# Performance work log

Measured on AMD Instinct MI355X. Metric: run time of the kernel, lower is better.

Reference implementation:

```python
import jax, jax.numpy as jnp
import numpy as np

# ---- constants from the source module ----
NB = [[0,1,2,3],[0,1,4],[0,2,5],[0,3,6],[1,4,7],[2,5,8],[3,6,9],[4,7,10],[5,8,11],[6,9],[7,10],[8,11],[12,13,14,15],[12,13,16],[12,14,17],[12,15],[13,16,18],[14,17,19],[16,18,20],[17,19,21],[18,20,22],[19,21,23],[20,22],[21,23]]
PARENT = np.array([0,0,0,0,1,2,3,4,5,6,7,8,9,9,9,12,13,14,16,17,18,19,20,21])  # root parent sentinel handled separately
KJ, NV, PREG = 24, 6890, 200
LEN = np.array([len(n) for n in NB])
NBR_IDX = np.zeros((KJ,4), np.int32)
NBR_VALID = np.zeros((KJ,4), np.float32)
for k, n in enumerate(NB):
    NBR_IDX[k,:len(n)] = n; NBR_VALID[k,:len(n)] = 1.0
BETA_POS = np.zeros((KJ,17), np.float32); BETA_POS[np.arange(KJ), 4*LEN] = 1.0
SLICE_MASK = np.zeros((23,17), np.float32)
for j in range(23):
    SLICE_MASK[j,:4*LEN[j]+1] = 1.0  # self.K[j] has 4*len(NB[j])+1 rows
NBR_IDX = jnp.asarray(NBR_IDX); NBR_VALID = jnp.asarray(NBR_VALID)
BETA_POS = jnp.asarray(BETA_POS); SLICE_MASK = jnpp = jnp.asarray(SLICE_MASK)


def setup_inputs() -> dict:
    key = jax.random.key(0)
    ks = jax.random.split(key, 9)
    V = jax.random.normal(ks[0], (PREG, NV, 3), jnp.float32)
    T = jax.random.normal(ks[1], (PREG, NV, 3), jnp.float32)
    J = jax.random.normal(ks[2], (PREG, KJ, 3), jnp.float32)
    theta = 0.3 * jax.random.normal(ks[3], (PREG, 72), jnp.float32)
    W_prime = jax.random.uniform(ks[4], (NV, KJ), jnp.float32)
    W_i = jax.random.uniform(ks[5], (NV, KJ), jnp.float32)
    W_i = W_i / W_i.sum(axis=1, keepdims=True)
    A = jax.random.uniform(ks[6], (23, NV), jnp.float32)
    K_mats = 0.01 * jax.random.normal(ks[7], (23, 17, 3 * NV), jnp.float32)
    K_mats = K_mats * SLICE_MASK[:, :, None]  # zero rows beyond the ragged per-joint size
    beta_2 = jnp.ones((1,), jnp.float32)
    return {"V": V, "T": T, "J": J, "theta": theta, "W_prime": W_prime, "W_i": W_i, "A": A, "K_mats": K_mats, "beta_2": beta_2, "epoch": 1}


def _rodrigues(pose):  # pose: (K,3)
    angle = jnp.maximum(jnp.linalg.norm(pose, axis=1, keepdims=True), 1e-8)
    axis = pose / angle
    x, y, z = axis[:, 0], axis[:, 1], axis[:, 2]
    zero = jnp.zeros_like(x)
    skew = jnp.stack([zero, -z, y, z, zero, -x, -y, x, zero], axis=1).reshape(-1, 3, 3)
    outer = axis[:, :, None] * axis[:, None, :]
    c = jnp.cos(angle)[:, :, None]
    s = jnp.sin(angle)[:, :, None]
    eye = jnp.eye(3, dtype=pose.dtype)[None]
    return c * eye + (1.0 - c) * outer + s * skew


def _compute_G(pose72, Jp):  # pose72: (72,), Jp: (K,3) -> (K,4,4)
    R = _rodrigues(pose72.reshape(KJ, 3))
    t = Jp - jnp.concatenate([jnp.zeros((1, 3), Jp.dtype), Jp[PARENT[1:]]], axis=0)
    G_local = jnp.zeros((KJ, 4, 4), Jp.dtype)
    G_local = G_local.at[:, :3, :3].set(R).at[:, :3, 3].set(t).at[:, 3, 3].set(1.0)
    Gs = [G_local[0]]
    for i in range(1, KJ):  # fixed 24-joint kinematic tree
        Gs.append(Gs[PARENT[i]] @ G_local[i])
    G = jnp.stack(Gs, axis=0)
    off = jnp.einsum('kij,kj->ki', G[:, :3, :3], Jp)  # homogeneous w=0 -> rotation only
    return G.at[:, :3, 3].add(-off)


def _axis2quat(p):  # (M,3) -> (M,4)
    angle = jnp.sqrt(jnp.maximum(jnp.sum(p ** 2, axis=1), 1e-16))
    n = p / angle[:, None]
    s = jnp.sin(angle / 2)
    return jnp.stack([n[:, 0] * s, n[:, 1] * s, n[:, 2] * s, jnp.cos(angle / 2) - 1.0], axis=1)


def reference(V, T, J, theta, W_prime, W_i, A, K_mats, beta_2, epoch):
    P = V.shape[0]
    b2 = beta_2[0]
    # normalized skinning weights
    W_relu = jax.nn.relu(W_prime)
    W_change = W_relu / (W_relu.sum(axis=1, keepdims=True) + 1e-8)
    # per-pose global joint transforms
    G_prime = jax.vmap(_compute_G)(theta, J)  # (P,K,4,4)
    # quaternion features and blend-shape correction
    q = _axis2quat(theta.reshape(P * KJ, 3)).reshape(P, KJ, 4)
    qg = q[:, NBR_IDX, :] * NBR_VALID[None, :, :, None]       # (P,K,4,4) neighbor gather
    q17 = jnp.concatenate([qg.reshape(P, KJ, 16), jnp.zeros((P, KJ, 1), q.dtype)], axis=-1)
    q17 = q17 + BETA_POS[None] * b2                            # beta_2 at column 4*len
    qm = q17[:, 1:, :] * SLICE_MASK[None]                      # ragged slice q_ne[:, j+1, :lenK]
    contrib = jnp.einsum('pjl,jlm->pjm', qm, K_mats).reshape(P, 23, NV, 3)
    T_p = jnp.einsum('pjnc,jn->pnc', contrib, jax.nn.relu(A)) + T
    # linear blend skinning
    T_h = jnp.concatenate([T_p, jnp.ones((P, NV, 1), T_p.dtype)], axis=-1)
    transformed = jnp.einsum('pkij,pnj->pnki', G_prime[:, :, :3, :], T_h)  # (P,N,K,3)
    verts = jnp.einsum('nk,pnkc->pnc', W_change, transformed)
    # energies
    e = float(epoch)
    g_wi = 0.1 * np.exp(-0.1 * e)
    g_w = 0.002 * np.exp(-0.008 * e)
    g_a = 0.001 * np.exp(-0.008 * e)
    g_k = 0.1 * np.exp(-0.008 * e)
    E_D = jnp.sum((V - verts) ** 2)
    E_Wi = jnp.sum((W_change - W_i) ** 2)
    E_W = jnp.sum(jnp.abs(W_change))
    E_A = jnp.sum(jnp.abs(A))
    E_K = jnp.sum(jnp.sqrt(jnp.sum(K_mats ** 2, axis=(1, 2))))
    E = E_D + g_wi * E_Wi + g_w * E_W + g_a * E_A + g_k * E_K
    return (E, verts)
```

## Files before the change

### kernel.cpp

```cpp
#include <hip/hip_runtime.h>
#include <math.h>

#define KJ 24
#define NV 6890
#define PREG 200
#define M_TOT (NV*3)
#define KDIM 391
#define KPAD 416
#define TP_STRIDE 20672
#define NMT64 323
#define NKB (NMT64*2)

#define EDP_OFF 0
#define EKP_OFF 5400
#define WIP_OFF 101984
#define EWP_OFF 102016
#define EAP_OFF 102048
#define RED_OFF 102080
#define G_OFF   102112
#define TP_OFF  159712
#define QBH_OFF_U 10903488
#define QBL_OFF_U 11009984
#define TP2_OFF 14157792

typedef __attribute__((ext_vector_type(8))) short short8;
typedef __attribute__((ext_vector_type(4))) float f32x4;
typedef __attribute__((ext_vector_type(4))) unsigned int u32x4;

__constant__ int c_PARENT[24] = {0,0,0,0,1,2,3,4,5,6,7,8,9,9,9,12,13,14,16,17,18,19,20,21};
__constant__ int c_DEPTH[24]  = {0,1,1,1,2,2,2,3,3,3,4,4,4,4,4,5,5,5,6,6,7,7,8,8};
__constant__ int c_LEN[24]    = {4,3,3,3,3,3,3,3,3,2,2,2,4,3,3,2,3,3,3,3,3,3,2,2};
__constant__ int c_NBR[24][4] = {
  {0,1,2,3},{0,1,4,0},{0,2,5,0},{0,3,6,0},{1,4,7,0},{2,5,8,0},{3,6,9,0},{4,7,10,0},
  {5,8,11,0},{6,9,0,0},{7,10,0,0},{8,11,0,0},{12,13,14,15},{12,13,16,0},{12,14,17,0},
  {12,15,0,0},{13,16,18,0},{14,17,19,0},{16,18,20,0},{17,19,21,0},{18,20,22,0},
  {19,21,23,0},{20,22,0,0},{21,23,0,0}};

__device__ __forceinline__ float waveReduce(float v) {
  #pragma unroll
  for (int off = 32; off > 0; off >>= 1) v += __shfl_down(v, off, 64);
  return v;
}
__device__ __forceinline__ unsigned short f2bf(float x) {
  union { float f; unsigned u; } v; v.f = x;
  unsigned r = v.u + 0x7FFFu + ((v.u >> 16) & 1u);
  return (unsigned short)(r >> 16);
}
__device__ __forceinline__ float bf2f(unsigned short h) {
  union { unsigned u; float f; } v; v.u = ((unsigned)h) << 16; return v.f;
}

__global__ __launch_bounds__(256) void kPre(const float* __restrict__ J,
                                            const float* __restrict__ theta,
                                            const float* __restrict__ beta2,
                                            const float* __restrict__ Wp,
                                            const float* __restrict__ Wi,
                                            const float* __restrict__ A,
                                            float* __restrict__ ws) {
  unsigned short* qbh = (unsigned short*)ws + QBH_OFF_U;
  unsigned short* qbl = (unsigned short*)ws + QBL_OFF_U;
  int b = blockIdx.x;
  if (b < 50) {
    __shared__ float Gl[4][24][12];
    __shared__ float Gg[4][24][12];
    __shared__ float q[4][24][4];
    int w = threadIdx.x >> 6, t = threadIdx.x & 63;
    int p = b*4 + w;
    if (t < 24) {
      float x = theta[p*72 + 3*t + 0];
      float y = theta[p*72 + 3*t + 1];
      float z = theta[p*72 + 3*t + 2];
      float n2 = x*x + y*y + z*z;
      float ang = fmaxf(sqrtf(n2), 1e-8f);
      float ia = 1.f/ang;
      float ax = x*ia, ay = y*ia, az = z*ia;
      float c = cosf(ang), s = sinf(ang), C = 1.f - c;
      float jx = J[p*72+3*t], jy = J[p*72+3*t+1], jz = J[p*72+3*t+2];
      float tx = jx, ty = jy, tz = jz;
      if (t > 0) {
        int par = c_PARENT[t];
        tx -= J[p*72+3*par]; ty -= J[p*72+3*par+1]; tz -= J[p*72+3*par+2];
      }
      Gl[w][t][0]=c+C*ax*ax;   Gl[w][t][1]=C*ax*ay-s*az; Gl[w][t][2]=C*ax*az+s*ay; Gl[w][t][3]=tx;
      Gl[w][t][4]=C*ax*ay+s*az;Gl[w][t][5]=c+C*ay*ay;    Gl[w][t][6]=C*ay*az-s*ax; Gl[w][t][7]=ty;
      Gl[w][t][8]=C*ax*az-s*ay;Gl[w][t][9]=C*ay*az+s*ax; Gl[w][t][10]=c+C*az*az;   Gl[w][t][11]=tz;
      float ang2 = sqrtf(fmaxf(n2, 1e-16f));
      float inv2 = 1.f/ang2;
      float s2 = sinf(0.5f*ang2);
      q[w][t][0] = x*inv2*s2; q[w][t][1] = y*inv2*s2; q[w][t][2] = z*inv2*s2;
      q[w][t][3] = cosf(0.5f*ang2) - 1.f;
    }
    __syncthreads();
    for (int lev = 0; lev <= 8; lev++) {
      if (t < 24 && c_DEPTH[t] == lev) {
        if (lev == 0) {
          for (int i2 = 0; i2 < 12; i2++) Gg[w][0][i2] = Gl[w][0][i2];
        } else {
          int par = c_PARENT[t];
          for (int r = 0; r < 3; r++) {
            float g0 = Gg[w][par][r*4+0], g1 = Gg[w][par][r*4+1];
            float g2 = Gg[w][par][r*4+2], g3 = Gg[w][par][r*4+3];
            for (int c2 = 0; c2 < 4; c2++) {
              float v = g0*Gl[w][t][0+c2] + g1*Gl[w][t][4+c2] + g2*Gl[w][t][8+c2];
              if (c2 == 3) v += g3;
              Gg[w][t][r*4+c2] = v;
            }
          }
        }
      }
      __syncthreads();
    }
    if (t < 24) {
      float jx = J[p*72+3*t], jy = J[p*72+3*t+1], jz = J[p*72+3*t+2];
      float* gp = ws + G_OFF + p*288 + t*12;
      #pragma unroll
      for (int r = 0; r < 3; r++) {
        float off = Gg[w][t][r*4+0]*jx + Gg[w][t][r*4+1]*jy + Gg[w][t][r*4+2]*jz;
        Gg[w][t][r*4+3] -= off;
      }
      #pragma unroll
      for (int i2 = 0; i2 < 12; i2++) gp[i2] = Gg[w][t][i2];
    }
    __syncthreads();
    float b2 = beta2[0];
    for (int e = t; e < KDIM; e += 64) {
      int j = e / 17, l = e - 17*j;
      int k = j + 1;
      float val = 0.f;
      if (l < 4*c_LEN[j] + 1) {
        if (l < 16) {
          int sidx = l >> 2, cc = l & 3;
          if (sidx < c_LEN[k]) val = q[w][c_NBR[k][sidx]][cc];
        }
        if (l == 4*c_LEN[k]) val += b2;
      }
      unsigned short hi = f2bf(val);
      unsigned short lo = f2bf(val - bf2f(hi));
      qbh[p*KPAD + e] = hi;
      qbl[p*KPAD + e] = lo;
    }
    for (int e = KDIM + t; e < KPAD; e += 64) {
      qbh[p*KPAD + e] = 0; qbl[p*KPAD + e] = 0;
    }
  } else {
    int d = b - 50;
    int t = threadIdx.x;
    int n = d*256 + t;
    float ewi = 0.f, ew = 0.f, ea = 0.f;
    if (n < NV) {
      float wv[24]; float sum = 0.f;
      const float4* wp4 = (const float4*)(Wp + n*24);
      #pragma unroll
      for (int i = 0; i < 6; i++) {
        float4 v4 = wp4[i];
        wv[4*i+0] = fmaxf(v4.x, 0.f); wv[4*i+1] = fmaxf(v4.y, 0.f);
        wv[4*i+2] = fmaxf(v4.z, 0.f); wv[4*i+3] = fmaxf(v4.w, 0.f);
        sum += wv[4*i+0]+wv[4*i+1]+wv[4*i+2]+wv[4*i+3];
      }
      float inv = 1.f/(sum + 1e-8f);
      #pragma unroll
      for (int k = 0; k < 24; k++) {
        float wc = wv[k]*inv;
        ew += fabsf(wc);
        float dd = wc - Wi[n*24+k];
        ewi += dd*dd;
      }
    }
    for (int i = d*256 + t; i < 23*NV; i += 27*256) ea += fabsf(A[i]);
    for (int i = d*256 + t; i < 56*KPAD; i += 27*256) {
      qbh[200*KPAD + i] = 0; qbl[200*KPAD + i] = 0;
    }
    __shared__ float red[3][4];
    int lane = t & 63, wv2 = t >> 6;
    ewi = waveReduce(ewi); ew = waveReduce(ew); ea = waveReduce(ea);
    if (lane == 0) { red[0][wv2] = ewi; red[1][wv2] = ew; red[2][wv2] = ea; }
    __syncthreads();
    if (t == 0) {
      ws[WIP_OFF + d] = red[0][0]+red[0][1]+red[0][2]+red[0][3];
      ws[EWP_OFF + d] = red[1][0]+red[1][1]+red[1][2]+red[1][3];
      ws[EAP_OFF + d] = red[2][0]+red[2][1]+red[2][2]+red[2][3];
    }
  }
}

template<int KS0, int NKS, int JMIN>
__device__ __forceinline__ void kb_body(const float* __restrict__ A,
                                        const float* __restrict__ K,
                                        const unsigned short* __restrict__ qbh,
                                        const unsigned short* __restrict__ qbl,
                                        float* __restrict__ Sk,
                                        short (*__restrict__ SBh)[64*32],
                                        short (*__restrict__ SBl)[64*32],
                                        float (*__restrict__ SA)[24],
                                        float* __restrict__ ek,
                                        float* __restrict__ ws,
                                        float* __restrict__ TPd,
                                        int m0, int flat) {
  const int tid = threadIdx.x;
  const int w = tid >> 6, lane = tid & 63;
  const int r = lane & 15, qd = lane >> 4;
  const int krow = tid >> 3, mseg = (tid & 7) * 8;
  const int mm = m0 + mseg;
  const int nb0 = m0 / 3;
  const int mrow2 = tid >> 2, kq2 = tid & 3;
  const int swr = ((mrow2 >> 4)*64 + kq2*16 + (mrow2 & 15)) * 8;

  if (tid < 23) ek[tid] = 0.f;
  for (int i = tid; i < 14*24; i += 256) {
    int jj = i / 24, nn = i - jj*24;
    int j2 = JMIN + jj, n2 = nb0 + nn;
    ((float*)SA)[i] = (j2 < 23 && n2 < NV) ? fmaxf(A[j2*NV + n2], 0.f) : 0.f;
  }

  f32x4 acc[4][4];
  #pragma unroll
  for (int h = 0; h < 4; h++)
    #pragma unroll
    for (int f = 0; f < 4; f++) acc[h][f] = (f32x4){0.f,0.f,0.f,0.f};

  int aofs[4];
  #pragma unroll
  for (int h = 0; h < 4; h++) aofs[h] = (w*64 + h*16 + r)*KPAD + KS0*32 + qd*8;

  short8 ah[2][4], al[2][4];
  float kv[8];

  auto loadK = [&](int ks) {
    int kg = (KS0 + ks)*32 + krow;
    #pragma unroll
    for (int i = 0; i < 8; i++) kv[i] = 0.f;
    if (kg < KDIM) {
      const float* kr = K + (size_t)kg*M_TOT + mm;
      if (mm + 7 < M_TOT) {
        float4 a4 = *(const float4*)kr; float4 b4 = *(const float4*)(kr+4);
        kv[0]=a4.x; kv[1]=a4.y; kv[2]=a4.z; kv[3]=a4.w;
        kv[4]=b4.x; kv[5]=b4.y; kv[6]=b4.z; kv[7]=b4.w;
      } else {
        #pragma unroll
        for (int i = 0; i < 8; i++) if (mm+i < M_TOT) kv[i] = kr[i];
      }
    }
  };
  auto stageK = [&](int ks) {
    int kg = (KS0 + ks)*32 + krow;
    float wv[8]; float sq = 0.f;
    #pragma unroll
    for (int i = 0; i < 8; i++) wv[i] = 0.f;
    if (kg < KDIM) {
      int jj = kg/17 - JMIN;
      int nb = mm / 3;
      float av[4];
      #pragma unroll
      for (int i = 0; i < 4; i++) av[i] = SA[jj][nb - nb0 + i];
      #pragma unroll
      for (int i = 0; i < 8; i++) {
        float a = (mm+i < M_TOT) ? av[(mm+i)/3 - nb] : 0.f;
        wv[i] = kv[i]*a;
        sq = fmaf(kv[i], kv[i], sq);
      }
    }
    #pragma unroll
    for (int c = 0; c < 4; c++)
      *(float2*)&Sk[krow*66 + mseg + 2*c] = make_float2(wv[2*c], wv[2*c+1]);
    sq += __shfl_xor(sq, 1, 64);
    sq += __shfl_xor(sq, 2, 64);
    sq += __shfl_xor(sq, 4, 64);
    if ((tid & 7) == 0 && kg < KDIM) atomicAdd(&ek[kg/17], sq);
  };
  auto xpose = [&](int buf) {
    float vv[8];
    #pragma unroll
    for (int j = 0; j < 8; j++) vv[j] = Sk[(kq2*8 + j)*66 + mrow2];
    unsigned dh[4], dl[4];
    #pragma unroll
    for (int c = 0; c < 4; c++) {
      unsigned short h0 = f2bf(vv[2*c]),   h1 = f2bf(vv[2*c+1]);
      unsigned short l0 = f2bf(vv[2*c]   - bf2f(h0));
      unsigned short l1 = f2bf(vv[2*c+1] - bf2f(h1));
      dh[c] = (unsigned)h0 | ((unsigned)h1 << 16);
      dl[c] = (unsigned)l0 | ((unsigned)l1 << 16);
    }
    *(u32x4*)&SBh[buf][swr] = (u32x4){dh[0], dh[1], dh[2], dh[3]};
    *(u32x4*)&SBl[buf][swr] = (u32x4){dl[0], dl[1], dl[2], dl[3]};
  };

  loadK(0);
  #pragma unroll
  for (int h = 0; h < 4; h++) {
    ah[0][h] = *(const short8*)(qbh + aofs[h]);
    al[0][h] = *(const short8*)(qbl + aofs[h]);
  }
  stageK(0);
  __syncthreads();
  xpose(0);
  #pragma unroll
  for (int h = 0; h < 4; h++) {
    ah[1][h] = *(const short8*)(qbh + aofs[h] + 32);
    al[1][h] = *(const short8*)(qbl + aofs[h] + 32);
  }
  __syncthreads();

  #pragma unroll
  for (int ks = 0; ks < NKS; ks++) {
    const int cur = ks & 1, nxt = cur ^ 1;
    if (ks + 1 < NKS) loadK(ks + 1);
    short8 bfh[4], bfl[4];
    #pragma unroll
    for (int f = 0; f < 4; f++) {
      bfh[f] = *(const short8*)&SBh[cur][(f*64 + lane)*8];
      bfl[f] = *(const short8*)&SBl[cur][(f*64 + lane)*8];
    }
    #pragma unroll
    for (int f = 0; f < 4; f++)
      #pragma unroll
      for (int h = 0; h < 4; h++) {
        acc[h][f] = __builtin_amdgcn_mfma_f32_16x16x32_bf16(ah[cur][h], bfh[f], acc[h][f], 0, 0, 0);
        acc[h][f] = __builtin_amdgcn_mfma_f32_16x16x32_bf16(ah[cur][h], bfl[f], acc[h][f], 0, 0, 0);
        acc[h][f] = __builtin_amdgcn_mfma_f32_16x16x32_bf16(al[cur][h], bfh[f], acc[h][f], 0, 0, 0);
      }
    if (ks + 1 < NKS) stageK(ks + 1);
    if (ks + 2 < NKS) {
      const int o = (ks + 2) * 32;
      #pragma unroll
      for (int h = 0; h < 4; h++) {
        ah[cur][h] = *(const short8*)(qbh + aofs[h] + o);
        al[cur][h] = *(const short8*)(qbl + aofs[h] + o);
      }
    }
    __syncthreads();
    if (ks + 1 < NKS) xpose(nxt);
    __syncthreads();
  }

  if (tid < 23) ws[EKP_OFF + tid*NKB + flat] = ek[tid];
  #pragma unroll
  for (int h = 0; h < 4; h++)
    #pragma unroll
    for (int f = 0; f < 4; f++)
      #pragma unroll
      for (int g = 0; g < 4; g++) {
        int p = w*64 + h*16 + qd*4 + g;
        if (p < PREG)
          TPd[(size_t)p*TP_STRIDE + m0 + f*16 + r] = acc[h][f][g];
      }
}

__global__ __launch_bounds__(256) void kB(const float* __restrict__ A,
                                          const float* __restrict__ K,
                                          float* __restrict__ ws) {
  __shared__ float Sk[32*66];
  __shared__ short SBh[2][64*32];
  __shared__ short SBl[2][64*32];
  __shared__ float SA[14][24];
  __shared__ float ek[23];
  const unsigned short* qbh = (const unsigned short*)ws + QBH_OFF_U;
  const unsigned short* qbl = (const unsigned short*)ws + QBL_OFF_U;
  const int m0 = blockIdx.x * 64;
  const int flat = blockIdx.x + blockIdx.y * NMT64;
  if (blockIdx.y == 0)
    kb_body<0, 7, 0>(A, K, qbh, qbl, Sk, SBh, SBl, SA, ek, ws, ws + TP_OFF,  m0, flat);
  else
    kb_body<7, 6, 13>(A, K, qbh, qbl, Sk, SBh, SBl, SA, ek, ws, ws + TP2_OFF, m0, flat);
}

__global__ __launch_bounds__(256) void kC(const float* __restrict__ V,
                                          const float* __restrict__ T,
                                          const float* __restrict__ Wp,
                                          const float* __restrict__ ws,
                                          float* __restrict__ out) {
  int p0 = blockIdx.y * 8;
  int n = blockIdx.x*256 + threadIdx.x;
  __shared__ float tmp[4];
  float ed = 0.f;
  if (n < NV) {
    float wv[24]; float sum = 0.f;
    const float4* wp4 = (const float4*)(Wp + n*24);
    #pragma unroll
    for (int i = 0; i < 6; i++) {
      float4 v4 = wp4[i];
      wv[4*i+0] = fmaxf(v4.x, 0.f); wv[4*i+1] = fmaxf(v4.y, 0.f);
      wv[4*i+2] = fmaxf(v4.z, 0.f); wv[4*i+3] = fmaxf(v4.w, 0.f);
      sum += wv[4*i+0]+wv[4*i+1]+wv[4*i+2]+wv[4*i+3];
    }
    float inv = 1.f/(sum + 1e-8f);
    for (int pp = 0; pp < 8; pp++) {
      int p = p0 + pp;
      const float* __restrict__ gp = ws + G_OFF + (size_t)p*288;
      float M[12];
      #pragma unroll
      for (int i = 0; i < 12; i++) M[i] = 0.f;
      #pragma unroll
      for (int k = 0; k < 24; k++) {
        float wc = wv[k];
        #pragma unroll
        for (int i = 0; i < 12; i++)
          M[i] = fmaf(wc, gp[k*12 + i], M[i]);
      }
      #pragma unroll
      for (int i = 0; i < 12; i++) M[i] *= inv;
      size_t tb = (size_t)p*M_TOT + 3*n;
      size_t pb = (size_t)p*TP_STRIDE + 3*n;
      float t0 = ws[TP_OFF + pb + 0] + ws[TP2_OFF + pb + 0] + T[tb + 0];
      float t1 = ws[TP_OFF + pb + 1] + ws[TP2_OFF + pb + 1] + T[tb + 1];
      float t2 = ws[TP_OFF + pb + 2] + ws[TP2_OFF + pb + 2] + T[tb + 2];
      float v0 = M[0]*t0 + M[1]*t1 + M[2]*t2  + M[3];
      float v1 = M[4]*t0 + M[5]*t1 + M[6]*t2  + M[7];
      float v2 = M[8]*t0 + M[9]*t1 + M[10]*t2 + M[11];
      out[1+tb+0] = v0; out[1+tb+1] = v1; out[1+tb+2] = v2;
      float d0 = V[tb+0]-v0, d1 = V[tb+1]-v1, d2 = V[tb+2]-v2;
      ed += d0*d0 + d1*d1 + d2*d2;
    }
  }
  ed = waveReduce(ed);
  int lane = threadIdx.x & 63, w = threadIdx.x >> 6;
  if (lane == 0) tmp[w] = ed;
  __syncthreads();
  if (threadIdx.x == 0)
    ((float*)ws)[EDP_OFF + blockIdx.y*27 + blockIdx.x] = tmp[0]+tmp[1]+tmp[2]+tmp[3];
}

__global__ __launch_bounds__(256) void kF1(float* __restrict__ ws) {
  __shared__ float sb[4];
  int b = blockIdx.x, t = threadIdx.x, lane = t & 63, w = t >> 6;
  if (b < 23) {
    float s = 0.f;
    for (int i = t; i < NKB; i += 256) s += ws[EKP_OFF + b*NKB + i];
    s = waveReduce(s);
    if (lane == 0) sb[w] = s;
    __syncthreads();
    if (t == 0) ws[RED_OFF + b] = sb[0]+sb[1]+sb[2]+sb[3];
  } else if (b == 23) {
    float s = 0.f;
    for (int i = t; i < 675; i += 256) s += ws[EDP_OFF + i];
    s = waveReduce(s);
    if (lane == 0) sb[w] = s;
    __syncthreads();
    if (t == 0) ws[RED_OFF + 23] = sb[0]+sb[1]+sb[2]+sb[3];
  } else {
    if (w == 0) {
      float s = (lane < 27) ? ws[WIP_OFF + lane] : 0.f;
      s = waveReduce(s);
      if (lane == 0) ws[RED_OFF + 24] = s;
    } else if (w == 1) {
      float s = (lane < 27) ? ws[EWP_OFF + lane] : 0.f;
      s = waveReduce(s);
      if (lane == 0) ws[RED_OFF + 25] = s;
    } else if (w == 2) {
      float s = (lane < 27) ? ws[EAP_OFF + lane] : 0.f;
      s = waveReduce(s);
      if (lane == 0) ws[RED_OFF + 26] = s;
    }
  }
}

__global__ void kF2(const int* __restrict__ epoch, const float* __restrict__ ws,
                    float* __restrict__ out) {
  int t = threadIdx.x;
  float s = (t < 23) ? sqrtf(ws[RED_OFF + t]) : 0.f;
  s = waveReduce(s);
  if (t == 0) {
    float e    = (float)epoch[0];
    float g_wi = 0.1f   * expf(-0.1f  * e);
    float g_w  = 0.002f * expf(-0.008f* e);
    float g_a  = 0.001f * expf(-0.008f* e);
    float g_k  = 0.1f   * expf(-0.008f* e);
    out[0] = ws[RED_OFF+23] + g_wi*ws[RED_OFF+24] + g_w*ws[RED_OFF+25]
           + g_a*ws[RED_OFF+26] + g_k*s;
  }
}

extern "C" void kernel_launch(void* const* d_in, const int* in_sizes, int n_in,
                              void* d_out, int out_size, void* d_ws, size_t ws_size,
                              hipStream_t stream) {
  const float* V     = (const float*)d_in[0];
  const float* T     = (const float*)d_in[1];
  const float* J     = (const float*)d_in[2];
  const float* theta = (const float*)d_in[3];
  const float* Wp    = (const float*)d_in[4];
  const float* Wi    = (const float*)d_in[5];
  const float* A     = (const float*)d_in[6];
  const float* K     = (const float*)d_in[7];
  const float* b2    = (const float*)d_in[8];
  const int*   epoch = (const int*)d_in[9];
  float* out = (float*)d_out;
  float* ws  = (float*)d_ws;

  hipLaunchKernelGGL(kPre, dim3(77),        dim3(256), 0, stream,
                     J, theta, b2, Wp, Wi, A, ws);
  hipLaunchKernelGGL(kB,   dim3(NMT64, 2),  dim3(256), 0, stream, A, K, ws);
  hipLaunchKernelGGL(kC,   dim3(27, 25),    dim3(256), 0, stream, V, T, Wp, ws, out);
  hipLaunchKernelGGL(kF1,  dim3(25),        dim3(256), 0, stream, ws);
  hipLaunchKernelGGL(kF2,  dim3(1),         dim3(64),  0, stream, epoch, ws, out);
}
```

Measured before the change: 175.6 us.

## Deepen kB pipeline with double-buffered staging and drop per-step barrier

The K-tile pipeline in kB becomes three stages deep: global loads run three steps ahead into a double-buffered register slot, staging runs two steps ahead into a double-buffered LDS scratch, and the transpose for the next step moves before the single remaining barrier, removing one __syncthreads per iteration. The per-joint norm accumulation no longer uses shared-memory atomics; each row's partial sum is written to LDS and reduced serially by 23 threads at the end. This costs more registers and LDS, which may lower occupancy, and the tail reduction loop is serial.

```diff
diff --git a/kernel.cpp b/kernel.cpp
--- a/kernel.cpp
+++ b/kernel.cpp
@@ -188,11 +188,11 @@
                                         const float* __restrict__ K,
                                         const unsigned short* __restrict__ qbh,
                                         const unsigned short* __restrict__ qbl,
-                                        float* __restrict__ Sk,
+                                        float (*__restrict__ Sk)[32*66],
                                         short (*__restrict__ SBh)[64*32],
                                         short (*__restrict__ SBl)[64*32],
                                         float (*__restrict__ SA)[24],
-                                        float* __restrict__ ek,
+                                        float* __restrict__ ek2,
                                         float* __restrict__ ws,
                                         float* __restrict__ TPd,
                                         int m0, int flat) {
@@ -205,7 +205,6 @@
   const int mrow2 = tid >> 2, kq2 = tid & 3;
   const int swr = ((mrow2 >> 4)*64 + kq2*16 + (mrow2 & 15)) * 8;
 
-  if (tid < 23) ek[tid] = 0.f;
   for (int i = tid; i < 14*24; i += 256) {
     int jj = i / 24, nn = i - jj*24;
     int j2 = JMIN + jj, n2 = nb0 + nn;
@@ -223,25 +222,27 @@
   for (int h = 0; h < 4; h++) aofs[h] = (w*64 + h*16 + r)*KPAD + KS0*32 + qd*8;
 
   short8 ah[2][4], al[2][4];
-  float kv[8];
+  float kv[2][8];
 
   auto loadK = [&](int ks) {
+    const int slot = ks & 1;
     int kg = (KS0 + ks)*32 + krow;
     #pragma unroll
-    for (int i = 0; i < 8; i++) kv[i] = 0.f;
+    for (int i = 0; i < 8; i++) kv[slot][i] = 0.f;
     if (kg < KDIM) {
       const float* kr = K + (size_t)kg*M_TOT + mm;
       if (mm + 7 < M_TOT) {
         float4 a4 = *(const float4*)kr; float4 b4 = *(const float4*)(kr+4);
-        kv[0]=a4.x; kv[1]=a4.y; kv[2]=a4.z; kv[3]=a4.w;
-        kv[4]=b4.x; kv[5]=b4.y; kv[6]=b4.z; kv[7]=b4.w;
+        kv[slot][0]=a4.x; kv[slot][1]=a4.y; kv[slot][2]=a4.z; kv[slot][3]=a4.w;
+        kv[slot][4]=b4.x; kv[slot][5]=b4.y; kv[slot][6]=b4.z; kv[slot][7]=b4.w;
       } else {
         #pragma unroll
-        for (int i = 0; i < 8; i++) if (mm+i < M_TOT) kv[i] = kr[i];
+        for (int i = 0; i < 8; i++) if (mm+i < M_TOT) kv[slot][i] = kr[i];
       }
     }
   };
   auto stageK = [&](int ks) {
+    const int slot = ks & 1;
     int kg = (KS0 + ks)*32 + krow;
     float wv[8]; float sq = 0.f;
     #pragma unroll
@@ -255,22 +256,23 @@
       #pragma unroll
       for (int i = 0; i < 8; i++) {
         float a = (mm+i < M_TOT) ? av[(mm+i)/3 - nb] : 0.f;
-        wv[i] = kv[i]*a;
-        sq = fmaf(kv[i], kv[i], sq);
+        wv[i] = kv[slot][i]*a;
+        sq = fmaf(kv[slot][i], kv[slot][i], sq);
       }
     }
     #pragma unroll
     for (int c = 0; c < 4; c++)
-      *(float2*)&Sk[krow*66 + mseg + 2*c] = make_float2(wv[2*c], wv[2*c+1]);
+      *(float2*)&Sk[slot][krow*66 + mseg + 2*c] = make_float2(wv[2*c], wv[2*c+1]);
     sq += __shfl_xor(sq, 1, 64);
     sq += __shfl_xor(sq, 2, 64);
     sq += __shfl_xor(sq, 4, 64);
-    if ((tid & 7) == 0 && kg < KDIM) atomicAdd(&ek[kg/17], sq);
+    if ((tid & 7) == 0) ek2[ks*32 + krow] = sq;
   };
-  auto xpose = [&](int buf) {
+  auto xpose = [&](int ks) {
+    const int slot = ks & 1;
     float vv[8];
     #pragma unroll
-    for (int j = 0; j < 8; j++) vv[j] = Sk[(kq2*8 + j)*66 + mrow2];
+    for (int j = 0; j < 8; j++) vv[j] = Sk[slot][(kq2*8 + j)*66 + mrow2];
     unsigned dh[4], dl[4];
     #pragma unroll
     for (int c = 0; c < 4; c++) {
@@ -280,8 +282,8 @@
       dh[c] = (unsigned)h0 | ((unsigned)h1 << 16);
       dl[c] = (unsigned)l0 | ((unsigned)l1 << 16);
     }
-    *(u32x4*)&SBh[buf][swr] = (u32x4){dh[0], dh[1], dh[2], dh[3]};
-    *(u32x4*)&SBl[buf][swr] = (u32x4){dl[0], dl[1], dl[2], dl[3]};
+    *(u32x4*)&SBh[slot][swr] = (u32x4){dh[0], dh[1], dh[2], dh[3]};
+    *(u32x4*)&SBl[slot][swr] = (u32x4){dl[0], dl[1], dl[2], dl[3]};
   };
 
   loadK(0);
@@ -291,8 +293,11 @@
     al[0][h] = *(const short8*)(qbl + aofs[h]);
   }
   stageK(0);
+  loadK(1);
   __syncthreads();
   xpose(0);
+  stageK(1);
+  loadK(2);
   #pragma unroll
   for (int h = 0; h < 4; h++) {
     ah[1][h] = *(const short8*)(qbh + aofs[h] + 32);
@@ -302,14 +307,14 @@
 
   #pragma unroll
   for (int ks = 0; ks < NKS; ks++) {
-    const int cur = ks & 1, nxt = cur ^ 1;
-    if (ks + 1 < NKS) loadK(ks + 1);
+    const int cur = ks & 1;
     short8 bfh[4], bfl[4];
     #pragma unroll
     for (int f = 0; f < 4; f++) {
       bfh[f] = *(const short8*)&SBh[cur][(f*64 + lane)*8];
       bfl[f] = *(const short8*)&SBl[cur][(f*64 + lane)*8];
     }
+    if (ks + 3 < NKS) loadK(ks + 3);
     #pragma unroll
     for (int f = 0; f < 4; f++)
       #pragma unroll
@@ -318,7 +323,8 @@
         acc[h][f] = __builtin_amdgcn_mfma_f32_16x16x32_bf16(ah[cur][h], bfl[f], acc[h][f], 0, 0, 0);
         acc[h][f] = __builtin_amdgcn_mfma_f32_16x16x32_bf16(al[cur][h], bfh[f], acc[h][f], 0, 0, 0);
       }
-    if (ks + 1 < NKS) stageK(ks + 1);
+    if (ks + 2 < NKS) stageK(ks + 2);
+    if (ks + 1 < NKS) xpose(ks + 1);
     if (ks + 2 < NKS) {
       const int o = (ks + 2) * 32;
       #pragma unroll
@@ -328,11 +334,16 @@
       }
     }
     __syncthreads();
-    if (ks + 1 < NKS) xpose(nxt);
-    __syncthreads();
-  }
-
-  if (tid < 23) ws[EKP_OFF + tid*NKB + flat] = ek[tid];
+  }
+
+  if (tid < 23) {
+    float s = 0.f;
+    for (int i2 = 0; i2 < NKS*32; i2++) {
+      int kg = KS0*32 + i2;
+      if (kg < KDIM && kg/17 == tid) s += ek2[i2];
+    }
+    ws[EKP_OFF + tid*NKB + flat] = s;
+  }
   #pragma unroll
   for (int h = 0; h < 4; h++)
     #pragma unroll
@@ -348,19 +359,19 @@
 __global__ __launch_bounds__(256) void kB(const float* __restrict__ A,
                                           const float* __restrict__ K,
                                           float* __restrict__ ws) {
-  __shared__ float Sk[32*66];
+  __shared__ float Sk[2][32*66];
   __shared__ short SBh[2][64*32];
   __shared__ short SBl[2][64*32];
   __shared__ float SA[14][24];
-  __shared__ float ek[23];
+  __shared__ float ek2[7*32];
   const unsigned short* qbh = (const unsigned short*)ws + QBH_OFF_U;
   const unsigned short* qbl = (const unsigned short*)ws + QBL_OFF_U;
   const int m0 = blockIdx.x * 64;
   const int flat = blockIdx.x + blockIdx.y * NMT64;
   if (blockIdx.y == 0)
-    kb_body<0, 7, 0>(A, K, qbh, qbl, Sk, SBh, SBl, SA, ek, ws, ws + TP_OFF,  m0, flat);
+    kb_body<0, 7, 0>(A, K, qbh, qbl, Sk, SBh, SBl, SA, ek2, ws, ws + TP_OFF,  m0, flat);
   else
-    kb_body<7, 6, 13>(A, K, qbh, qbl, Sk, SBh, SBl, SA, ek, ws, ws + TP2_OFF, m0, flat);
+    kb_body<7, 6, 13>(A, K, qbh, qbl, Sk, SBh, SBl, SA, ek2, ws, ws + TP2_OFF, m0, flat);
 }
 
 __global__ __launch_bounds__(256) void kC(const float* __restrict__ V,
```

Result: slower. 214.8 us (+22.3%).
